# Performance work log

Measured on AMD Instinct MI355X. Metric: run time of the kernel, lower is better.

Reference implementation:

```python
import jax, jax.numpy as jnp
import numpy as np

DIM = 1024
NUM_EXPERTS = 8
TOP_K = 2


def setup_inputs() -> dict:
    key = jax.random.key(0)
    ks = jax.random.split(key, 7)
    s_in = 1.0 / np.sqrt(DIM)
    s_hid = 1.0 / np.sqrt(4 * DIM)
    x = jax.random.normal(ks[0], (2, 2048, DIM), dtype=jnp.float32)
    gate_w = jax.random.normal(ks[1], (DIM, NUM_EXPERTS), dtype=jnp.float32) * s_in
    gate_b = jax.random.normal(ks[2], (NUM_EXPERTS,), dtype=jnp.float32) * 0.01
    w1 = jax.random.normal(ks[3], (NUM_EXPERTS, DIM, 4 * DIM), dtype=jnp.float32) * s_in
    b1 = jax.random.normal(ks[4], (NUM_EXPERTS, 4 * DIM), dtype=jnp.float32) * 0.01
    w2 = jax.random.normal(ks[5], (NUM_EXPERTS, 4 * DIM, DIM), dtype=jnp.float32) * s_hid
    b2 = jax.random.normal(ks[6], (NUM_EXPERTS, DIM), dtype=jnp.float32) * 0.01
    return {"x": x, "gate_w": gate_w, "gate_b": gate_b, "w1": w1, "b1": b1, "w2": w2, "b2": b2}


def reference(x, gate_w, gate_b, w1, b1, w2, b2):
    # Faithful to the torch module in EVAL mode (no routing noise).
    # Quirks reproduced: (1) gather of expert inputs degenerates to flat_x
    # (all top_k copies identical); (2) softmax-normalized gates are dead code
    # (never applied); (3) the per-expert masked assignment overwrites all
    # TOP_K. Net: out = TOP_K * FFN_{max(topk_idx)}(x).
    B, N, C = x.shape
    flat_x = x.reshape(-1, C)                      # [T, C]
    logits = flat_x @ gate_w + gate_b              # [T, E]
    _, topk_idx = jax.lax.top_k(logits, TOP_K)     # [T, k]
    e_star = jnp.max(topk_idx, axis=-1)            # [T] last-overwriting expert
    out = jnp.zeros_like(flat_x)
    for i in range(NUM_EXPERTS):                   # fixed small expert loop
        h = jax.nn.gelu(flat_x @ w1[i] + b1[i], approximate=False)  # exact GELU (torch default)
        y = h @ w2[i] + b2[i]                      # [T, C]
        out = jnp.where((e_star == i)[:, None], y, out)
    return (TOP_K * out).reshape(B, N, C)
```

## Files before the change

kernel.cpp:

```cpp
#include <hip/hip_runtime.h>
#include <hip/hip_bf16.h>
#include <hip/hip_fp16.h>

#define T_TOKENS 4096
#define DIMC 1024
#define HID 4096
#define NE 8

typedef _Float16 f16;
typedef _Float16 f16x8 __attribute__((ext_vector_type(8)));
typedef _Float16 f16x4 __attribute__((ext_vector_type(4)));
typedef float f32x4 __attribute__((ext_vector_type(4)));

__device__ __forceinline__ void gload_lds16(const f16* g, f16* l) {
    __builtin_amdgcn_global_load_lds(
        (const __attribute__((address_space(1))) void*)g,
        (__attribute__((address_space(3))) void*)l, 16, 0, 0);
}

__global__ __launch_bounds__(256) void gating_kernel(
    const float* __restrict__ x, const float* __restrict__ gw,
    const float* __restrict__ gb, int* __restrict__ counts,
    int* __restrict__ list, int* __restrict__ eidx)
{
    const int wave = threadIdx.x >> 6;
    const int lane = threadIdx.x & 63;
    const int t = blockIdx.x * 4 + wave;

    const float* xr = x + (size_t)t * DIMC;
    float acc[NE];
#pragma unroll
    for (int e = 0; e < NE; ++e) acc[e] = 0.f;

    for (int i = 0; i < DIMC / 64; ++i) {
        const int k = i * 64 + lane;
        const float xv = xr[k];
        const float* g = gw + (size_t)k * NE;
#pragma unroll
        for (int e = 0; e < NE; ++e) acc[e] = fmaf(xv, g[e], acc[e]);
    }
#pragma unroll
    for (int off = 32; off >= 1; off >>= 1) {
#pragma unroll
        for (int e = 0; e < NE; ++e) acc[e] += __shfl_xor(acc[e], off, 64);
    }
    if (lane == 0) {
        float lg[NE];
#pragma unroll
        for (int e = 0; e < NE; ++e) lg[e] = acc[e] + gb[e];
        int i1 = 0; float v1 = lg[0];
#pragma unroll
        for (int e = 1; e < NE; ++e) { if (lg[e] > v1) { v1 = lg[e]; i1 = e; } }
        int i2 = -1; float v2 = -3.4e38f;
#pragma unroll
        for (int e = 0; e < NE; ++e) {
            if (e == i1) continue;
            if (lg[e] > v2) { v2 = lg[e]; i2 = e; }
        }
        const int es = (i1 > i2) ? i1 : i2;
        const int pos = atomicAdd(&counts[es], 1);
        list[es * T_TOKENS + pos] = t;
        eidx[t] = es;
    }
}

__global__ __launch_bounds__(256) void xconvert(const float* __restrict__ x,
                                                f16* __restrict__ xh)
{
    const size_t i = ((size_t)blockIdx.x * 256 + threadIdx.x) * 8;
    const float4 a = *(const float4*)(x + i);
    const float4 b = *(const float4*)(x + i + 4);
    f16x8 v;
    v[0] = (f16)a.x; v[1] = (f16)a.y; v[2] = (f16)a.z; v[3] = (f16)a.w;
    v[4] = (f16)b.x; v[5] = (f16)b.y; v[6] = (f16)b.z; v[7] = (f16)b.w;
    *(f16x8*)(xh + i) = v;
}

__global__ __launch_bounds__(256) void wconvert(const float* __restrict__ W,
                                                f16* __restrict__ Wt,
                                                int K, int N)
{
    __shared__ f16 Lt[64 * 72];
    const int n0 = blockIdx.x * 64;
    const int k0 = blockIdx.y * 64;
    const float* Ws = W + (size_t)blockIdx.z * K * N;
    const int t = threadIdx.x;

    const int no = (t & 15) * 4;
    const int kr = t >> 4;
#pragma unroll
    for (int p = 0; p < 4; ++p) {
        const int k = kr + p * 16;
        const float4 v = *(const float4*)(Ws + (size_t)(k0 + k) * N + n0 + no);
        Lt[(no + 0) * 72 + k] = (f16)v.x;
        Lt[(no + 1) * 72 + k] = (f16)v.y;
        Lt[(no + 2) * 72 + k] = (f16)v.z;
        Lt[(no + 3) * 72 + k] = (f16)v.w;
    }
    __syncthreads();
    const int n = t >> 2;
    const int ko = (t & 3) * 16;
    const f16x8 a = *(const f16x8*)&Lt[n * 72 + ko];
    const f16x8 b = *(const f16x8*)&Lt[n * 72 + ko + 8];
    f16* dst = Wt + ((size_t)blockIdx.z * N + n0 + n) * K + k0 + ko;
    *(f16x8*)(dst) = a;
    *(f16x8*)(dst + 8) = b;
}

template <bool FIRST>
__global__ __launch_bounds__(512) void ffn_gemm9(
    const f16* __restrict__ A, const f16* __restrict__ Bt,
    const int* __restrict__ counts, const int* __restrict__ list,
    f16* __restrict__ Pout)
{
    constexpr int KB   = FIRST ? DIMC : HID;
    constexpr int NTOT = FIRST ? HID : DIMC;
    constexpr int NKT  = 16;

    const int zz  = blockIdx.z;
    const int e   = FIRST ? (zz >> 1) : (zz >> 3);
    const int ks  = FIRST ? (zz & 1) : (zz & 7);
    const int kk0 = ks * 512;
    const int m0  = blockIdx.y * 128;
    const int n0  = blockIdx.x * 256;
    const int cnt = counts[e];
    if (m0 >= cnt) return;

    __shared__ __align__(16) f16 As[128 * 32];
    __shared__ __align__(16) f16 Bs[256 * 32];
    __shared__ int rows[128];

    const int tid = threadIdx.x;
    if (tid < 128) rows[tid] = (m0 + tid < cnt) ? list[e * T_TOKENS + m0 + tid] : -1;
    __syncthreads();

    const int lane = tid & 63;
    const int wv   = tid >> 6;
    const int wr   = wv >> 2;
    const int wc   = wv & 3;

    const int lrow4 = lane >> 2;
    const int lslot = lane & 3;

    const int arow = wv * 16 + lrow4;
    int tokA = rows[arow]; if (tokA < 0) tokA = 0;
    const int achunk = lslot ^ (((arow >> 2) ^ arow) & 3);
    const f16* asrc = A + (size_t)tokA * KB + kk0 + achunk * 8;
    f16* adst = As + (wv * 16) * 32;

    const f16* bsrc[2];
    f16* bdst[2];
#pragma unroll
    for (int j = 0; j < 2; ++j) {
        const int brow = wv * 32 + j * 16 + lrow4;
        const int bchunk = lslot ^ (((brow >> 2) ^ brow) & 3);
        bsrc[j] = Bt + ((size_t)e * NTOT + n0 + brow) * KB + kk0 + bchunk * 8;
        bdst[j] = Bs + (wv * 32 + j * 16) * 32;
    }

    f32x4 acc[4][4];
#pragma unroll
    for (int mi = 0; mi < 4; ++mi)
#pragma unroll
        for (int ni = 0; ni < 4; ++ni) acc[mi][ni] = f32x4{0.f, 0.f, 0.f, 0.f};

    for (int kt = 0; kt < NKT; ++kt) {
        const int ko = kt * 32;
        __syncthreads();
        gload_lds16(asrc + ko, adst);
        gload_lds16(bsrc[0] + ko, bdst[0]);
        gload_lds16(bsrc[1] + ko, bdst[1]);
        __syncthreads();
        {
            f16x8 af[4], bf[4];
            const int slot = lane >> 4;
#pragma unroll
            for (int mi = 0; mi < 4; ++mi) {
                const int row = wr * 64 + mi * 16 + (lane & 15);
                const int kb  = (slot ^ (((row >> 2) ^ row) & 3)) << 4;
                af[mi] = *(const f16x8*)((const char*)As + row * 64 + kb);
            }
#pragma unroll
            for (int ni = 0; ni < 4; ++ni) {
                const int n  = wc * 64 + ni * 16 + (lane & 15);
                const int kb = (slot ^ (((n >> 2) ^ n) & 3)) << 4;
                bf[ni] = *(const f16x8*)((const char*)Bs + n * 64 + kb);
            }
#pragma unroll
            for (int mi = 0; mi < 4; ++mi)
#pragma unroll
                for (int ni = 0; ni < 4; ++ni)
                    acc[mi][ni] = __builtin_amdgcn_mfma_f32_16x16x32_f16(
                        af[mi], bf[ni], acc[mi][ni], 0, 0, 0);
        }
    }

    constexpr int NOUT = FIRST ? HID : DIMC;
#pragma unroll
    for (int ni = 0; ni < 4; ++ni) {
        const int gc = n0 + wc * 64 + ni * 16 + (lane & 15);
#pragma unroll
        for (int mi = 0; mi < 4; ++mi) {
#pragma unroll
            for (int r = 0; r < 4; ++r) {
                const int lrow = wr * 64 + mi * 16 + (lane >> 4) * 4 + r;
                const int tok = rows[lrow];
                if (tok < 0) continue;
                Pout[((size_t)ks * T_TOKENS + tok) * NOUT + gc] =
                    (f16)acc[mi][ni][r];
            }
        }
    }
}

__global__ __launch_bounds__(256) void gelu_combine(
    const f16* __restrict__ Hp, const float* __restrict__ b1,
    const int* __restrict__ eidx, f16* __restrict__ H)
{
    const size_t i = ((size_t)blockIdx.x * 256 + threadIdx.x) * 8;
    const int t = (int)(i >> 12);
    const int c = (int)(i & (HID - 1));
    const int e = eidx[t];
    const f16x8 a = *(const f16x8*)(Hp + i);
    const f16x8 b = *(const f16x8*)(Hp + (size_t)T_TOKENS * HID + i);
    const float4 ba = *(const float4*)(b1 + (size_t)e * HID + c);
    const float4 bb = *(const float4*)(b1 + (size_t)e * HID + c + 4);
    const float bj[8] = {ba.x, ba.y, ba.z, ba.w, bb.x, bb.y, bb.z, bb.w};
    f16x8 o;
#pragma unroll
    for (int j = 0; j < 8; ++j) {
        const float v = (float)a[j] + (float)b[j] + bj[j];
        o[j] = (f16)(0.5f * v * (1.f + erff(v * 0.70710678118f)));
    }
    *(f16x8*)(H + i) = o;
}

__global__ __launch_bounds__(256) void reduce8(
    const f16* __restrict__ p8, const float* __restrict__ b2,
    const int* __restrict__ eidx, float* __restrict__ out)
{
    constexpr size_t SL = (size_t)T_TOKENS * DIMC;
    const size_t i = ((size_t)blockIdx.x * 256 + threadIdx.x) * 8;
    const int t = (int)(i >> 10);
    const int c = (int)(i & (DIMC - 1));
    const int e = eidx[t];
    float s[8] = {0.f, 0.f, 0.f, 0.f, 0.f, 0.f, 0.f, 0.f};
#pragma unroll
    for (int ks = 0; ks < 8; ++ks) {
        const f16x8 v = *(const f16x8*)(p8 + (size_t)ks * SL + i);
#pragma unroll
        for (int j = 0; j < 8; ++j) s[j] += (float)v[j];
    }
    const float4 ba = *(const float4*)(b2 + (size_t)e * DIMC + c);
    const float4 bb = *(const float4*)(b2 + (size_t)e * DIMC + c + 4);
    const float bj[8] = {ba.x, ba.y, ba.z, ba.w, bb.x, bb.y, bb.z, bb.w};
    float4 o0, o1;
    o0.x = 2.f * (s[0] + bj[0]); o0.y = 2.f * (s[1] + bj[1]);
    o0.z = 2.f * (s[2] + bj[2]); o0.w = 2.f * (s[3] + bj[3]);
    o1.x = 2.f * (s[4] + bj[4]); o1.y = 2.f * (s[5] + bj[5]);
    o1.z = 2.f * (s[6] + bj[6]); o1.w = 2.f * (s[7] + bj[7]);
    *(float4*)(out + i) = o0;
    *(float4*)(out + i + 4) = o1;
}

template <bool FIRST>
__global__ __launch_bounds__(256) void ffn_gemm_fb(
    const float* __restrict__ x, const f16* __restrict__ Hin,
    const float* __restrict__ w1, const float* __restrict__ b1,
    const float* __restrict__ w2, const float* __restrict__ b2,
    const int* __restrict__ counts, const int* __restrict__ list,
    f16* __restrict__ Hout, float* __restrict__ out)
{
    constexpr int K = FIRST ? DIMC : HID;
    constexpr int N = FIRST ? HID : DIMC;
    constexpr int LDT = 40;

    const int e  = blockIdx.z;
    const int m0 = blockIdx.y * 128;
    const int n0 = blockIdx.x * 128;
    const int cnt = counts[e];
    if (m0 >= cnt) return;

    __shared__ f16 Ab[128 * LDT];
    __shared__ f16 Bb[128 * LDT];
    __shared__ int rows[128];

    const int tid = threadIdx.x;
    if (tid < 128) {
        const int p = m0 + tid;
        rows[tid] = (p < cnt) ? list[e * T_TOKENS + p] : -1;
    }
    __syncthreads();

    const int lane = tid & 63;
    const int wv = tid >> 6;
    const int wr = wv >> 1, wc = wv & 1;

    f32x4 acc[4][4];
#pragma unroll
    for (int mi = 0; mi < 4; ++mi)
#pragma unroll
        for (int ni = 0; ni < 4; ++ni) acc[mi][ni] = f32x4{0.f, 0.f, 0.f, 0.f};

    const float* Bsrc = (FIRST ? w1 : w2) + (size_t)e * K * N;

    for (int kk = 0; kk < K; kk += 32) {
        __syncthreads();
        {
            const int r  = tid >> 3;
            const int ko = (tid & 7) * 4;
#pragma unroll
            for (int p = 0; p < 4; ++p) {
                const int row = p * 32 + r;
                const int tok = rows[row];
                f16x4 hv;
                if (FIRST) {
                    float4 v;
                    if (tok >= 0) v = *(const float4*)(x + (size_t)tok * K + kk + ko);
                    else          v = make_float4(0.f, 0.f, 0.f, 0.f);
                    hv[0] = (f16)v.x; hv[1] = (f16)v.y; hv[2] = (f16)v.z; hv[3] = (f16)v.w;
                } else {
                    if (tok >= 0) hv = *(const f16x4*)(Hin + (size_t)tok * K + kk + ko);
                    else { hv[0] = (f16)0.f; hv[1] = (f16)0.f; hv[2] = (f16)0.f; hv[3] = (f16)0.f; }
                }
                *(f16x4*)&Ab[row * LDT + ko] = hv;
            }
        }
        {
            const int kb = tid >> 5;
            const int no = (tid & 31) * 4;
#pragma unroll
            for (int p = 0; p < 4; ++p) {
                const int k = p * 8 + kb;
                const float4 v = *(const float4*)(Bsrc + (size_t)(kk + k) * N + n0 + no);
                f16 h[4];
                h[0] = (f16)v.x; h[1] = (f16)v.y; h[2] = (f16)v.z; h[3] = (f16)v.w;
#pragma unroll
                for (int i = 0; i < 4; ++i) {
                    const int n = no + i;
                    const int chunk = (k >> 3) ^ ((n >> 2) & 3);
                    Bb[n * LDT + chunk * 8 + (k & 7)] = h[i];
                }
            }
        }
        __syncthreads();
        f16x8 af[4], bf[4];
#pragma unroll
        for (int mi = 0; mi < 4; ++mi) {
            const int row = wr * 64 + mi * 16 + (lane & 15);
            af[mi] = *(const f16x8*)&Ab[row * LDT + (lane >> 4) * 8];
        }
#pragma unroll
        for (int ni = 0; ni < 4; ++ni) {
            const int n = wc * 64 + ni * 16 + (lane & 15);
            const int chunk = (lane >> 4) ^ ((n >> 2) & 3);
            bf[ni] = *(const f16x8*)&Bb[n * LDT + chunk * 8];
        }
#pragma unroll
        for (int mi = 0; mi < 4; ++mi)
#pragma unroll
            for (int ni = 0; ni < 4; ++ni)
                acc[mi][ni] = __builtin_amdgcn_mfma_f32_16x16x32_f16(
                    af[mi], bf[ni], acc[mi][ni], 0, 0, 0);
    }

#pragma unroll
    for (int ni = 0; ni < 4; ++ni) {
        const int gc = n0 + wc * 64 + ni * 16 + (lane & 15);
        const float bias = FIRST ? b1[(size_t)e * HID + gc]
                                 : b2[(size_t)e * DIMC + gc];
#pragma unroll
        for (int mi = 0; mi < 4; ++mi) {
#pragma unroll
            for (int r = 0; r < 4; ++r) {
                const int lrow = wr * 64 + mi * 16 + (lane >> 4) * 4 + r;
                const int tok = rows[lrow];
                if (tok < 0) continue;
                const float v = acc[mi][ni][r] + bias;
                if (FIRST) {
                    const float g = 0.5f * v * (1.f + erff(v * 0.70710678118f));
                    Hout[(size_t)tok * HID + gc] = (f16)g;
                } else {
                    out[(size_t)tok * DIMC + gc] = 2.f * v;
                }
            }
        }
    }
}

extern "C" void kernel_launch(void* const* d_in, const int* in_sizes, int n_in,
                              void* d_out, int out_size, void* d_ws, size_t ws_size,
                              hipStream_t stream)
{
    const float* x   = (const float*)d_in[0];
    const float* gw  = (const float*)d_in[1];
    const float* gb  = (const float*)d_in[2];
    const float* w1  = (const float*)d_in[3];
    const float* b1  = (const float*)d_in[4];
    const float* w2  = (const float*)d_in[5];
    const float* b2  = (const float*)d_in[6];
    float* out = (float*)d_out;

    const size_t MB = 1 << 20;
    const size_t need_p = 233 * MB;

    if (ws_size >= need_p) {
        int* counts = (int*)d_ws;
        int* list   = (int*)((char*)d_ws + 1024);
        int* eidx   = (int*)((char*)d_ws + 512 * 1024);
        f16* xh     = (f16*)((char*)d_ws + 1 * MB);
        f16* H      = (f16*)((char*)d_ws + 9 * MB);
        f16* w1t    = (f16*)((char*)d_ws + 41 * MB);
        f16* w2t    = (f16*)((char*)d_ws + 105 * MB);
        f16* Hp     = (f16*)((char*)d_ws + 169 * MB);
        f16* p8     = (f16*)((char*)d_ws + 169 * MB);

        hipMemsetAsync(counts, 0, 1024, stream);

        gating_kernel<<<T_TOKENS / 4, 256, 0, stream>>>(x, gw, gb, counts, list, eidx);
        xconvert<<<(T_TOKENS * DIMC) / (256 * 8), 256, 0, stream>>>(x, xh);
        wconvert<<<dim3(HID / 64, DIMC / 64, NE), 256, 0, stream>>>(w1, w1t, DIMC, HID);
        wconvert<<<dim3(DIMC / 64, HID / 64, NE), 256, 0, stream>>>(w2, w2t, HID, DIMC);

        ffn_gemm9<true><<<dim3(HID / 256, T_TOKENS / 128, NE * 2), 512, 0, stream>>>(
            xh, w1t, counts, list, Hp);
        gelu_combine<<<(T_TOKENS * HID) / (256 * 8), 256, 0, stream>>>(Hp, b1, eidx, H);
        ffn_gemm9<false><<<dim3(DIMC / 256, T_TOKENS / 128, NE * 8), 512, 0, stream>>>(
            H, w2t, counts, list, p8);
        reduce8<<<(T_TOKENS * DIMC) / (256 * 8), 256, 0, stream>>>(p8, b2, eidx, out);
        return;
    }

    const size_t need_fb = (size_t)(1 << 18) + (size_t)T_TOKENS * HID * sizeof(f16);
    if (ws_size < need_fb) return;

    int* counts = (int*)d_ws;
    int* list   = (int*)((char*)d_ws + 1024);
    int* eidx   = (int*)((char*)d_ws + 160 * 1024);
    f16* H      = (f16*)((char*)d_ws + (1 << 18));

    hipMemsetAsync(d_ws, 0, 1024, stream);
    gating_kernel<<<T_TOKENS / 4, 256, 0, stream>>>(x, gw, gb, counts, list, eidx);
    ffn_gemm_fb<true><<<dim3(HID / 128, T_TOKENS / 128, NE), 256, 0, stream>>>(
        x, (const f16*)nullptr, w1, b1, w2, b2, counts, list, H, out);
    ffn_gemm_fb<false><<<dim3(DIMC / 128, T_TOKENS / 128, NE), 256, 0, stream>>>(
        x, (const f16*)H, w1, b1, w2, b2, counts, list, H, out);
}
```

Measured before the change: 341.4 us.

## Merge prep kernels and overlap w2 conversion with first expert GEMM

Gating, x conversion and w1 transpose-conversion are merged into one launch that dispatches on block index. The w2 conversion moves into extra z-slices of the first GEMM grid, so it runs alongside the first GEMM's blocks. The intent is to remove launch gaps and tail idle time between the small preprocessing kernels. In exchange the GEMM blocks now use a shared memory buffer sized for the conversion path, and the mixed grid may schedule less evenly.

```diff
diff --git a/kernel.cpp b/kernel.cpp
--- a/kernel.cpp
+++ b/kernel.cpp
@@ -18,20 +18,19 @@
         (__attribute__((address_space(3))) void*)l, 16, 0, 0);
 }
 
-__global__ __launch_bounds__(256) void gating_kernel(
-    const float* __restrict__ x, const float* __restrict__ gw,
+__device__ __forceinline__ void gating_body(
+    int bid, int tid, const float* __restrict__ x, const float* __restrict__ gw,
     const float* __restrict__ gb, int* __restrict__ counts,
     int* __restrict__ list, int* __restrict__ eidx)
 {
-    const int wave = threadIdx.x >> 6;
-    const int lane = threadIdx.x & 63;
-    const int t = blockIdx.x * 4 + wave;
+    const int wave = tid >> 6;
+    const int lane = tid & 63;
+    const int t = bid * 4 + wave;
 
     const float* xr = x + (size_t)t * DIMC;
     float acc[NE];
 #pragma unroll
     for (int e = 0; e < NE; ++e) acc[e] = 0.f;
-
     for (int i = 0; i < DIMC / 64; ++i) {
         const int k = i * 64 + lane;
         const float xv = xr[k];
@@ -64,10 +63,10 @@
     }
 }
 
-__global__ __launch_bounds__(256) void xconvert(const float* __restrict__ x,
-                                                f16* __restrict__ xh)
-{
-    const size_t i = ((size_t)blockIdx.x * 256 + threadIdx.x) * 8;
+__device__ __forceinline__ void xconvert_body(
+    int bid, int tid, const float* __restrict__ x, f16* __restrict__ xh)
+{
+    const size_t i = ((size_t)bid * 256 + tid) * 8;
     const float4 a = *(const float4*)(x + i);
     const float4 b = *(const float4*)(x + i + 4);
     f16x8 v;
@@ -76,16 +75,13 @@
     *(f16x8*)(xh + i) = v;
 }
 
-__global__ __launch_bounds__(256) void wconvert(const float* __restrict__ W,
-                                                f16* __restrict__ Wt,
-                                                int K, int N)
-{
-    __shared__ f16 Lt[64 * 72];
-    const int n0 = blockIdx.x * 64;
-    const int k0 = blockIdx.y * 64;
-    const float* Ws = W + (size_t)blockIdx.z * K * N;
-    const int t = threadIdx.x;
-
+__device__ __forceinline__ void wconv_tile(
+    const float* __restrict__ W, f16* __restrict__ Wt, int K, int N,
+    int bx, int by, int bz, int t, f16* Lt)
+{
+    const int n0 = bx * 64;
+    const int k0 = by * 64;
+    const float* Ws = W + (size_t)bz * K * N;
     const int no = (t & 15) * 4;
     const int kr = t >> 4;
 #pragma unroll
@@ -102,35 +98,71 @@
     const int ko = (t & 3) * 16;
     const f16x8 a = *(const f16x8*)&Lt[n * 72 + ko];
     const f16x8 b = *(const f16x8*)&Lt[n * 72 + ko + 8];
-    f16* dst = Wt + ((size_t)blockIdx.z * N + n0 + n) * K + k0 + ko;
+    f16* dst = Wt + ((size_t)bz * N + n0 + n) * K + k0 + ko;
     *(f16x8*)(dst) = a;
     *(f16x8*)(dst + 8) = b;
 }
 
-template <bool FIRST>
-__global__ __launch_bounds__(512) void ffn_gemm9(
+__global__ __launch_bounds__(256) void prep_kernel(
+    const float* __restrict__ x, const float* __restrict__ gw,
+    const float* __restrict__ gb, const float* __restrict__ w1,
+    int* __restrict__ counts, int* __restrict__ list, int* __restrict__ eidx,
+    f16* __restrict__ xh, f16* __restrict__ w1t)
+{
+    __shared__ f16 Lt[64 * 72];
+    const int bid = blockIdx.x;
+    const int tid = threadIdx.x;
+    if (bid < 1024) {
+        gating_body(bid, tid, x, gw, gb, counts, list, eidx);
+    } else if (bid < 1024 + 2048) {
+        xconvert_body(bid - 1024, tid, x, xh);
+    } else {
+        const int t2 = bid - 3072;
+        const int bx = t2 & 63;
+        const int by = (t2 >> 6) & 15;
+        const int bz = t2 >> 10;
+        wconv_tile(w1, w1t, DIMC, HID, bx, by, bz, tid, Lt);
+    }
+}
+
+__global__ __launch_bounds__(512) void gemm1_wc2(
     const f16* __restrict__ A, const f16* __restrict__ Bt,
+    const float* __restrict__ w2, f16* __restrict__ w2t,
     const int* __restrict__ counts, const int* __restrict__ list,
     f16* __restrict__ Pout)
 {
-    constexpr int KB   = FIRST ? DIMC : HID;
-    constexpr int NTOT = FIRST ? HID : DIMC;
+    __shared__ __align__(16) char smem[25088];
+    const int tid = threadIdx.x;
+    const int zz  = blockIdx.z;
+
+    if (zz >= 16) {
+        const int s = blockIdx.x + blockIdx.y * 16 + (zz - 16) * 512;
+        const int h = tid >> 8;
+        const int t = s * 2 + h;
+        const int bx = t & 15;
+        const int by = (t >> 4) & 63;
+        const int bz = t >> 10;
+        f16* Lt = (f16*)smem + h * (64 * 72);
+        wconv_tile(w2, w2t, HID, DIMC, bx, by, bz, tid & 255, Lt);
+        return;
+    }
+
+    constexpr int KB   = DIMC;
+    constexpr int NTOT = HID;
     constexpr int NKT  = 16;
 
-    const int zz  = blockIdx.z;
-    const int e   = FIRST ? (zz >> 1) : (zz >> 3);
-    const int ks  = FIRST ? (zz & 1) : (zz & 7);
+    const int e   = zz >> 1;
+    const int ks  = zz & 1;
     const int kk0 = ks * 512;
     const int m0  = blockIdx.y * 128;
     const int n0  = blockIdx.x * 256;
     const int cnt = counts[e];
     if (m0 >= cnt) return;
 
-    __shared__ __align__(16) f16 As[128 * 32];
-    __shared__ __align__(16) f16 Bs[256 * 32];
-    __shared__ int rows[128];
-
-    const int tid = threadIdx.x;
+    f16* As = (f16*)smem;
+    f16* Bs = (f16*)(smem + 8192);
+    int* rows = (int*)(smem + 8192 + 16384);
+
     if (tid < 128) rows[tid] = (m0 + tid < cnt) ? list[e * T_TOKENS + m0 + tid] : -1;
     __syncthreads();
 
@@ -195,7 +227,6 @@
         }
     }
 
-    constexpr int NOUT = FIRST ? HID : DIMC;
 #pragma unroll
     for (int ni = 0; ni < 4; ++ni) {
         const int gc = n0 + wc * 64 + ni * 16 + (lane & 15);
@@ -206,7 +237,111 @@
                 const int lrow = wr * 64 + mi * 16 + (lane >> 4) * 4 + r;
                 const int tok = rows[lrow];
                 if (tok < 0) continue;
-                Pout[((size_t)ks * T_TOKENS + tok) * NOUT + gc] =
+                Pout[((size_t)ks * T_TOKENS + tok) * HID + gc] =
+                    (f16)acc[mi][ni][r];
+            }
+        }
+    }
+}
+
+__global__ __launch_bounds__(512) void ffn_gemm9b(
+    const f16* __restrict__ A, const f16* __restrict__ Bt,
+    const int* __restrict__ counts, const int* __restrict__ list,
+    f16* __restrict__ Pout)
+{
+    constexpr int KB   = HID;
+    constexpr int NTOT = DIMC;
+    constexpr int NKT  = 16;
+
+    const int zz  = blockIdx.z;
+    const int e   = zz >> 3;
+    const int ks  = zz & 7;
+    const int kk0 = ks * 512;
+    const int m0  = blockIdx.y * 128;
+    const int n0  = blockIdx.x * 256;
+    const int cnt = counts[e];
+    if (m0 >= cnt) return;
+
+    __shared__ __align__(16) f16 As[128 * 32];
+    __shared__ __align__(16) f16 Bs[256 * 32];
+    __shared__ int rows[128];
+
+    const int tid = threadIdx.x;
+    if (tid < 128) rows[tid] = (m0 + tid < cnt) ? list[e * T_TOKENS + m0 + tid] : -1;
+    __syncthreads();
+
+    const int lane = tid & 63;
+    const int wv   = tid >> 6;
+    const int wr   = wv >> 2;
+    const int wc   = wv & 3;
+
+    const int lrow4 = lane >> 2;
+    const int lslot = lane & 3;
+
+    const int arow = wv * 16 + lrow4;
+    int tokA = rows[arow]; if (tokA < 0) tokA = 0;
+    const int achunk = lslot ^ (((arow >> 2) ^ arow) & 3);
+    const f16* asrc = A + (size_t)tokA * KB + kk0 + achunk * 8;
+    f16* adst = As + (wv * 16) * 32;
+
+    const f16* bsrc[2];
+    f16* bdst[2];
+#pragma unroll
+    for (int j = 0; j < 2; ++j) {
+        const int brow = wv * 32 + j * 16 + lrow4;
+        const int bchunk = lslot ^ (((brow >> 2) ^ brow) & 3);
+        bsrc[j] = Bt + ((size_t)e * NTOT + n0 + brow) * KB + kk0 + bchunk * 8;
+        bdst[j] = Bs + (wv * 32 + j * 16) * 32;
+    }
+
+    f32x4 acc[4][4];
+#pragma unroll
+    for (int mi = 0; mi < 4; ++mi)
+#pragma unroll
+        for (int ni = 0; ni < 4; ++ni) acc[mi][ni] = f32x4{0.f, 0.f, 0.f, 0.f};
+
+    for (int kt = 0; kt < NKT; ++kt) {
+        const int ko = kt * 32;
+        __syncthreads();
+        gload_lds16(asrc + ko, adst);
+        gload_lds16(bsrc[0] + ko, bdst[0]);
+        gload_lds16(bsrc[1] + ko, bdst[1]);
+        __syncthreads();
+        {
+            f16x8 af[4], bf[4];
+            const int slot = lane >> 4;
+#pragma unroll
+            for (int mi = 0; mi < 4; ++mi) {
+                const int row = wr * 64 + mi * 16 + (lane & 15);
+                const int kb  = (slot ^ (((row >> 2) ^ row) & 3)) << 4;
+                af[mi] = *(const f16x8*)((const char*)As + row * 64 + kb);
+            }
+#pragma unroll
+            for (int ni = 0; ni < 4; ++ni) {
+                const int n  = wc * 64 + ni * 16 + (lane & 15);
+                const int kb = (slot ^ (((n >> 2) ^ n) & 3)) << 4;
+                bf[ni] = *(const f16x8*)((const char*)Bs + n * 64 + kb);
+            }
+#pragma unroll
+            for (int mi = 0; mi < 4; ++mi)
+#pragma unroll
+                for (int ni = 0; ni < 4; ++ni)
+                    acc[mi][ni] = __builtin_amdgcn_mfma_f32_16x16x32_f16(
+                        af[mi], bf[ni], acc[mi][ni], 0, 0, 0);
+        }
+    }
+
+#pragma unroll
+    for (int ni = 0; ni < 4; ++ni) {
+        const int gc = n0 + wc * 64 + ni * 16 + (lane & 15);
+#pragma unroll
+        for (int mi = 0; mi < 4; ++mi) {
+#pragma unroll
+            for (int r = 0; r < 4; ++r) {
+                const int lrow = wr * 64 + mi * 16 + (lane >> 4) * 4 + r;
+                const int tok = rows[lrow];
+                if (tok < 0) continue;
+                Pout[((size_t)ks * T_TOKENS + tok) * DIMC + gc] =
                     (f16)acc[mi][ni][r];
             }
         }
@@ -388,6 +523,14 @@
     }
 }
 
+__global__ __launch_bounds__(256) void gating_fb(
+    const float* __restrict__ x, const float* __restrict__ gw,
+    const float* __restrict__ gb, int* __restrict__ counts,
+    int* __restrict__ list, int* __restrict__ eidx)
+{
+    gating_body(blockIdx.x, threadIdx.x, x, gw, gb, counts, list, eidx);
+}
+
 extern "C" void kernel_launch(void* const* d_in, const int* in_sizes, int n_in,
                               void* d_out, int out_size, void* d_ws, size_t ws_size,
                               hipStream_t stream)
@@ -417,16 +560,17 @@
 
         hipMemsetAsync(counts, 0, 1024, stream);
 
-        gating_kernel<<<T_TOKENS / 4, 256, 0, stream>>>(x, gw, gb, counts, list, eidx);
-        xconvert<<<(T_TOKENS * DIMC) / (256 * 8), 256, 0, stream>>>(x, xh);
-        wconvert<<<dim3(HID / 64, DIMC / 64, NE), 256, 0, stream>>>(w1, w1t, DIMC, HID);
-        wconvert<<<dim3(DIMC / 64, HID / 64, NE), 256, 0, stream>>>(w2, w2t, HID, DIMC);
-
-        ffn_gemm9<true><<<dim3(HID / 256, T_TOKENS / 128, NE * 2), 512, 0, stream>>>(
-            xh, w1t, counts, list, Hp);
+        prep_kernel<<<1024 + 2048 + 8192, 256, 0, stream>>>(
+            x, gw, gb, w1, counts, list, eidx, xh, w1t);
+
+        gemm1_wc2<<<dim3(16, 32, 24), 512, 0, stream>>>(
+            xh, w1t, w2, w2t, counts, list, Hp);
+
         gelu_combine<<<(T_TOKENS * HID) / (256 * 8), 256, 0, stream>>>(Hp, b1, eidx, H);
-        ffn_gemm9<false><<<dim3(DIMC / 256, T_TOKENS / 128, NE * 8), 512, 0, stream>>>(
+
+        ffn_gemm9b<<<dim3(DIMC / 256, T_TOKENS / 128, NE * 8), 512, 0, stream>>>(
             H, w2t, counts, list, p8);
+
         reduce8<<<(T_TOKENS * DIMC) / (256 * 8), 256, 0, stream>>>(p8, b2, eidx, out);
         return;
     }
@@ -440,7 +584,7 @@
     f16* H      = (f16*)((char*)d_ws + (1 << 18));
 
     hipMemsetAsync(d_ws, 0, 1024, stream);
-    gating_kernel<<<T_TOKENS / 4, 256, 0, stream>>>(x, gw, gb, counts, list, eidx);
+    gating_fb<<<T_TOKENS / 4, 256, 0, stream>>>(x, gw, gb, counts, list, eidx);
     ffn_gemm_fb<true><<<dim3(HID / 128, T_TOKENS / 128, NE), 256, 0, stream>>>(
         x, (const f16*)nullptr, w1, b1, w2, b2, counts, list, H, out);
     ffn_gemm_fb<false><<<dim3(DIMC / 128, T_TOKENS / 128, NE), 256, 0, stream>>>(
```

New measurement: 313.7 us (median of 2 runs). -8.1%, faster.
